# Performance work log

Hardware: AMD Instinct MI355X
Metric: run time of the kernel (lower is better)

The kernel has to match this reference:

```python
import jax, jax.numpy as jnp
import numpy as np

BN_EPS = 1e-5
COS_EPS = 1e-6
LEAKY_SLOPE = 0.01
SIMILARITY_RATIO = 0.5


def setup_inputs() -> dict:
    key = jax.random.key(0)
    ks = jax.random.split(key, 5)
    B, D2, D, M = 2048, 256, 128, 100000
    item_feature = jax.random.normal(ks[0], (B, D2), dtype=jnp.float32)
    all_items = jax.random.normal(ks[1], (M, D), dtype=jnp.float32)
    user_item_id = jax.random.randint(ks[2], (B, 2), 0, M, dtype=jnp.int64)
    W = jax.random.normal(ks[3], (D2, D), dtype=jnp.float32) * (1.0 / np.sqrt(D2))
    b = jax.random.normal(ks[4], (D,), dtype=jnp.float32) * 0.01
    gamma = jnp.ones((D,), dtype=jnp.float32)
    beta = jnp.zeros((D,), dtype=jnp.float32)
    return {"item_feature": item_feature, "all_items": all_items,
            "user_item_id": user_item_id, "W": W, "b": b,
            "gamma": gamma, "beta": beta}


def reference(item_feature, all_items, user_item_id, W, b, gamma, beta):
    # Linear -> BatchNorm1d (training-mode batch stats, biased var) -> LeakyReLU
    h = item_feature @ W + b                       # [B, D]
    mu = jnp.mean(h, axis=0)
    var = jnp.var(h, axis=0)
    hn = (h - mu) * jax.lax.rsqrt(var + BN_EPS) * gamma + beta
    uf = jnp.where(hn >= 0, hn, LEAKY_SLOPE * hn)  # leaky relu

    # dense scoring + top-1 retrieval: [B, M] score matrix
    scores = uf @ all_items.T
    top1 = jnp.argmax(scores, axis=1)              # [B]

    # gather original and retrieved item embeddings
    orig = user_item_id[:, 1]
    a = all_items[orig]                            # [B, D]
    c = all_items[top1]                            # [B, D]

    # cosine similarity (torch CosineSimilarity semantics, eps=1e-6)
    na = jnp.maximum(jnp.sqrt(jnp.sum(a * a, axis=1)), COS_EPS)
    nc = jnp.maximum(jnp.sqrt(jnp.sum(c * c, axis=1)), COS_EPS)
    sim = jnp.sum(a * c, axis=1) / (na * nc)
    sim = (sim + 1.0) * 0.5                        # regularize to [0,1]

    # margin loss against constant labels = similarity_ratio
    labels = jnp.full(sim.shape, SIMILARITY_RATIO, dtype=sim.dtype)
    similarity_loss = jnp.mean(jnp.maximum(sim - labels, 0.0))

    return top1, similarity_loss, jnp.mean(sim)
```

## Files before the change

kernel.cpp:

```cpp
#include <hip/hip_runtime.h>
#include <stdint.h>

#define B_ROWS 2048
#define D2_DIM 256
#define D_DIM 128
#define M_ITEMS 100000
#define M_PAD 100352
#define BN_EPS_F 1e-5f
#define COS_EPS_F 1e-6f
#define LEAKY_F 0.01f

#define BNI 128
#define BK 32
#define SUPER 4

typedef __bf16 bf16x8 __attribute__((ext_vector_type(8)));
typedef float f32x4 __attribute__((ext_vector_type(4)));

__device__ unsigned short g_Aph[B_ROWS * D_DIM];
__device__ unsigned short g_Apl[B_ROWS * D_DIM];
__device__ unsigned short g_Bph[M_PAD * D_DIM];
__device__ unsigned short g_Bpl[M_PAD * D_DIM];

__device__ __forceinline__ unsigned bf16_rne(float f) {
  unsigned u = __float_as_uint(f);
  return (u + 0x7fffu + ((u >> 16) & 1u)) >> 16;
}
__device__ __forceinline__ void split_bf16(float v, unsigned short& hi, unsigned short& lo) {
  unsigned h = bf16_rne(v);
  float hf = __uint_as_float(h << 16);
  unsigned l = bf16_rne(v - hf);
  hi = (unsigned short)h; lo = (unsigned short)l;
}
__device__ __forceinline__ void gload16(const void* g, void* l) {
  __builtin_amdgcn_global_load_lds(
      (const __attribute__((address_space(1))) void*)g,
      (__attribute__((address_space(3))) void*)l, 16, 0, 0);
}

__global__ void k_gemm1(const float* __restrict__ A, const float* __restrict__ W,
                        const float* __restrict__ bias, float* __restrict__ h) {
  __shared__ float arow[D2_DIM];
  const int r = blockIdx.x;
  const int c = threadIdx.x;
  arow[c] = A[r * D2_DIM + c];
  arow[c + 128] = A[r * D2_DIM + c + 128];
  __syncthreads();
  float acc = 0.f;
#pragma unroll 8
  for (int k = 0; k < D2_DIM; k++) acc = fmaf(arow[k], W[k * D_DIM + c], acc);
  h[r * D_DIM + c] = acc + bias[c];
}

__global__ void k_bnstats(const float* __restrict__ h, const float* __restrict__ gamma,
                          const float* __restrict__ beta, float* __restrict__ scale,
                          float* __restrict__ shift) {
  const int c = blockIdx.x;
  const int t = threadIdx.x;
  double s = 0.0, sq = 0.0;
  for (int r = t; r < B_ROWS; r += 256) {
    double v = (double)h[r * D_DIM + c];
    s += v; sq += v * v;
  }
  __shared__ double ls[256], lq[256];
  ls[t] = s; lq[t] = sq;
  __syncthreads();
  for (int off = 128; off; off >>= 1) {
    if (t < off) { ls[t] += ls[t + off]; lq[t] += lq[t + off]; }
    __syncthreads();
  }
  if (t == 0) {
    double mean = ls[0] / (double)B_ROWS;
    double var = lq[0] / (double)B_ROWS - mean * mean;
    float sc = (float)((double)gamma[c] / sqrt(var + (double)BN_EPS_F));
    scale[c] = sc;
    shift[c] = beta[c] - (float)mean * sc;
  }
}

__global__ void k_norm_split(const float* __restrict__ h, const float* __restrict__ scale,
                             const float* __restrict__ shift) {
  int i = blockIdx.x * 256 + threadIdx.x;
  if (i >= B_ROWS * D_DIM) return;
  int c = i & (D_DIM - 1);
  float v = fmaf(h[i], scale[c], shift[c]);
  v = v >= 0.f ? v : LEAKY_F * v;
  unsigned short hi, lo;
  split_bf16(v, hi, lo);
  g_Aph[i] = hi; g_Apl[i] = lo;
}

__global__ void k_build_items(const float* __restrict__ items) {
  long long t = (long long)blockIdx.x * 256 + threadIdx.x;
  long long base = t * 4;
  if (base >= (long long)M_PAD * D_DIM) return;
  float4 v;
  if (base < (long long)M_ITEMS * D_DIM) v = *(const float4*)&items[base];
  else v = make_float4(0.f, 0.f, 0.f, 0.f);
  ushort4 hv, lv;
  split_bf16(v.x, hv.x, lv.x);
  split_bf16(v.y, hv.y, lv.y);
  split_bf16(v.z, hv.z, lv.z);
  split_bf16(v.w, hv.w, lv.w);
  *(ushort4*)&g_Bph[base] = hv;
  *(ushort4*)&g_Bpl[base] = lv;
}

__global__ void k_init(unsigned long long* __restrict__ keys) {
  int i = blockIdx.x * blockDim.x + threadIdx.x;
  if (i < B_ROWS) keys[i] = 0ull;
}

__launch_bounds__(256, 2)
__global__ void k_scores_mfma(unsigned long long* __restrict__ keys) {
  __shared__ __align__(16) char smem[81920];
  char* bufs[3] = { smem, smem + 16384, smem + 32768 };
  char* sAlo = smem + 49152;

  const int tid = threadIdx.x;
  const int l = tid & 63;
  const int w = tid >> 6;
  const int wm = w >> 1;
  const int wn = w & 1;
  const int rowbase = blockIdx.x * 128;
  const int chunk = blockIdx.y * (SUPER * BNI);
  const int lrow = l & 15;
  const int lkg = l >> 4;

  auto STAGEB = [&](int itembase, int ks, char* buf) {
#pragma unroll
    for (int rep = 0; rep < 2; rep++) {
      const int s = tid + rep * 256;
      const size_t goff = (size_t)(itembase + (s >> 2)) * D_DIM + ks
                        + ((s & 3) ^ ((s >> 3) & 3)) * 8;
      gload16(g_Bph + goff, buf + s * 16);
      gload16(g_Bpl + goff, buf + 8192 + s * 16);
    }
  };

#pragma unroll
  for (int rep = 0; rep < 8; rep++) {
    const int s = tid + rep * 256;
    gload16(g_Apl + (size_t)(rowbase + (s >> 4)) * D_DIM
                  + ((s & 15) ^ ((s >> 4) & 15)) * 8,
            sAlo + s * 16);
  }
  bf16x8 ah[4][4];
  {
    const int ar = rowbase + wm * 64 + lrow;
#pragma unroll
    for (int mi = 0; mi < 4; mi++)
#pragma unroll
      for (int kf = 0; kf < 4; kf++)
        ah[mi][kf] = *(const bf16x8*)&g_Aph[(size_t)(ar + mi * 16) * D_DIM + kf * 32 + lkg * 8];
  }
  STAGEB(chunk, 0, bufs[0]);
  STAGEB(chunk, BK, bufs[1]);

  float bestv[16];
  int besti[16];
#pragma unroll
  for (int q = 0; q < 16; q++) { bestv[q] = -3.0e38f; besti[q] = 0x7fffffff; }

  f32x4 acc[4][4];
#pragma unroll
  for (int mi = 0; mi < 4; mi++)
#pragma unroll
    for (int ni = 0; ni < 4; ni++) acc[mi][ni] = (f32x4)(0.0f);

#pragma unroll
  for (int s = 0; s < SUPER; s++) {
    const int itembase = chunk + s * BNI;
#pragma unroll
    for (int kf = 0; kf < 4; kf++) {
      const int j = s * 4 + kf;
      asm volatile("s_waitcnt vmcnt(4)" ::: "memory");
      __builtin_amdgcn_s_barrier();
      {
        const int q = j + 2;
        const int qt = (q >> 2) & (SUPER - 1);
        STAGEB(chunk + qt * BNI, (q & 3) * BK, bufs[q % 3]);
      }
      char* buf = bufs[j % 3];
      bf16x8 bh[4], bl[4], alo[4];
#pragma unroll
      for (int ni = 0; ni < 4; ni++) {
        const int item = wn * 64 + ni * 16 + lrow;
        const int off = (item * 4 + (lkg ^ ((item >> 1) & 3))) * 16;
        bh[ni] = *(const bf16x8*)(buf + off);
        bl[ni] = *(const bf16x8*)(buf + 8192 + off);
      }
#pragma unroll
      for (int mi = 0; mi < 4; mi++) {
        const int row = wm * 64 + mi * 16 + lrow;
        const int off = row * 256 + (((kf * 4 + lkg) ^ (row & 15)) << 4);
        alo[mi] = *(const bf16x8*)(sAlo + off);
      }
      __builtin_amdgcn_s_setprio(1);
#pragma unroll
      for (int mi = 0; mi < 4; mi++)
#pragma unroll
        for (int ni = 0; ni < 4; ni++) {
          f32x4 c = acc[mi][ni];
          c = __builtin_amdgcn_mfma_f32_16x16x32_bf16(ah[mi][kf], bh[ni], c, 0, 0, 0);
          c = __builtin_amdgcn_mfma_f32_16x16x32_bf16(alo[mi], bh[ni], c, 0, 0, 0);
          c = __builtin_amdgcn_mfma_f32_16x16x32_bf16(ah[mi][kf], bl[ni], c, 0, 0, 0);
          acc[mi][ni] = c;
        }
      __builtin_amdgcn_s_setprio(0);
    }
#pragma unroll
    for (int mi = 0; mi < 4; mi++)
#pragma unroll
      for (int ni = 0; ni < 4; ni++) {
        const int col = itembase + wn * 64 + ni * 16 + lrow;
        const bool valid = col < M_ITEMS;
#pragma unroll
        for (int reg = 0; reg < 4; reg++) {
          const float v = acc[mi][ni][reg];
          const int q = mi * 4 + reg;
          if (valid && v > bestv[q]) { bestv[q] = v; besti[q] = col; }
        }
        acc[mi][ni] = (f32x4)(0.0f);
      }
  }
  asm volatile("s_waitcnt vmcnt(0)" ::: "memory");

#pragma unroll
  for (int q = 0; q < 16; q++) {
    float v = bestv[q];
    int bi = besti[q];
#pragma unroll
    for (int off = 1; off < 16; off <<= 1) {
      float ov = __shfl_xor(v, off, 16);
      int oi = __shfl_xor(bi, off, 16);
      if (ov > v || (ov == v && oi < bi)) { v = ov; bi = oi; }
    }
    if (lrow == 0) {
      const int row = rowbase + wm * 64 + (q >> 2) * 16 + lkg * 4 + (q & 3);
      unsigned u = __float_as_uint(v);
      u = (u & 0x80000000u) ? ~u : (u | 0x80000000u);
      unsigned long long key =
          ((unsigned long long)u << 32) | (unsigned)(~(unsigned)bi);
      atomicMax(&keys[row], key);
    }
  }
}

__global__ void k_post(const unsigned long long* __restrict__ keys,
                       const int* __restrict__ uid,
                       const float* __restrict__ items,
                       float* __restrict__ out, float* __restrict__ sims,
                       float* __restrict__ rl) {
  int r = blockIdx.x * blockDim.x + threadIdx.x;
  if (r >= B_ROWS) return;
  unsigned long long key = keys[r];
  int idx = (int)(~(unsigned)(key & 0xFFFFFFFFull));
  out[r] = (float)idx;
  int orig = uid[2 * r + 1];
  const float* a = items + (long long)orig * D_DIM;
  const float* c = items + (long long)idx * D_DIM;
  float aa = 0.f, cc = 0.f, ac = 0.f;
#pragma unroll 4
  for (int d = 0; d < D_DIM; d++) {
    float x = a[d], y = c[d];
    aa = fmaf(x, x, aa);
    cc = fmaf(y, y, cc);
    ac = fmaf(x, y, ac);
  }
  float na = fmaxf(sqrtf(aa), COS_EPS_F);
  float nc = fmaxf(sqrtf(cc), COS_EPS_F);
  float sim = ac / (na * nc);
  sim = (sim + 1.f) * 0.5f;
  sims[r] = sim;
  rl[r] = fmaxf(sim - 0.5f, 0.f);
}

__global__ void k_final(const float* __restrict__ sims, const float* __restrict__ rl,
                        float* __restrict__ out) {
  __shared__ float s1[256], s2[256];
  int t = threadIdx.x;
  float a = 0.f, b = 0.f;
  for (int r = t; r < B_ROWS; r += 256) { a += rl[r]; b += sims[r]; }
  s1[t] = a; s2[t] = b;
  __syncthreads();
  for (int off = 128; off; off >>= 1) {
    if (t < off) { s1[t] += s1[t + off]; s2[t] += s2[t + off]; }
    __syncthreads();
  }
  if (t == 0) {
    out[B_ROWS] = s1[0] / (float)B_ROWS;
    out[B_ROWS + 1] = s2[0] / (float)B_ROWS;
  }
}

extern "C" void kernel_launch(void* const* d_in, const int* in_sizes, int n_in,
                              void* d_out, int out_size, void* d_ws, size_t ws_size,
                              hipStream_t stream) {
  const float* item_feature = (const float*)d_in[0];
  const float* all_items    = (const float*)d_in[1];
  const int*   uid          = (const int*)d_in[2];
  const float* W            = (const float*)d_in[3];
  const float* bias         = (const float*)d_in[4];
  const float* gamma        = (const float*)d_in[5];
  const float* beta         = (const float*)d_in[6];
  float* out = (float*)d_out;

  float* h     = (float*)d_ws;
  float* scale = h + B_ROWS * D_DIM;
  float* shift = scale + D_DIM;
  unsigned long long* keys = (unsigned long long*)(shift + D_DIM);
  float* sims  = (float*)(keys + B_ROWS);
  float* rl    = sims + B_ROWS;

  k_gemm1<<<B_ROWS, D_DIM, 0, stream>>>(item_feature, W, bias, h);
  k_bnstats<<<D_DIM, 256, 0, stream>>>(h, gamma, beta, scale, shift);
  k_norm_split<<<(B_ROWS * D_DIM + 255) / 256, 256, 0, stream>>>(h, scale, shift);
  k_build_items<<<(M_PAD * D_DIM / 4 + 255) / 256, 256, 0, stream>>>(all_items);
  k_init<<<(B_ROWS + 255) / 256, 256, 0, stream>>>(keys);
  dim3 sg(B_ROWS / 128, M_PAD / (SUPER * BNI));
  k_scores_mfma<<<sg, 256, 0, stream>>>(keys);
  k_post<<<(B_ROWS + 255) / 256, 256, 0, stream>>>(keys, uid, all_items, out, sims, rl);
  k_final<<<1, 256, 0, stream>>>(sims, rl, out);
}
```

Measured before the change: 282.8 us.

## Switch to double-buffered 64-wide K stages and load A-low directly from global

The B-tile pipeline changes from a triple buffer with 32-wide K steps and a partial vmcnt wait to a double buffer with 64-wide K steps and a full vmcnt(0) wait before each barrier. The A low-part tile is no longer kept in LDS; it is reloaded from global memory (cache) every step into registers. The intent is to halve the barrier count, cut LDS use so more can stay resident, and raise work per stage. In exchange, prefetch overlap is shallower because every stage waits for all outstanding loads, and the per-step global A loads add latency and register pressure.

```diff
diff --git a/kernel.cpp b/kernel.cpp
--- a/kernel.cpp
+++ b/kernel.cpp
@@ -11,8 +11,9 @@
 #define LEAKY_F 0.01f
 
 #define BNI 128
-#define BK 32
+#define BKS 64
 #define SUPER 4
+#define NSTEPS 8
 
 typedef __bf16 bf16x8 __attribute__((ext_vector_type(8)));
 typedef float f32x4 __attribute__((ext_vector_type(4)));
@@ -113,9 +114,8 @@
 
 __launch_bounds__(256, 2)
 __global__ void k_scores_mfma(unsigned long long* __restrict__ keys) {
-  __shared__ __align__(16) char smem[81920];
-  char* bufs[3] = { smem, smem + 16384, smem + 32768 };
-  char* sAlo = smem + 49152;
+  __shared__ __align__(16) char smem[65536];
+  char* bufs[2] = { smem, smem + 32768 };
 
   const int tid = threadIdx.x;
   const int l = tid & 63;
@@ -129,33 +129,23 @@
 
   auto STAGEB = [&](int itembase, int ks, char* buf) {
 #pragma unroll
-    for (int rep = 0; rep < 2; rep++) {
+    for (int rep = 0; rep < 4; rep++) {
       const int s = tid + rep * 256;
-      const size_t goff = (size_t)(itembase + (s >> 2)) * D_DIM + ks
-                        + ((s & 3) ^ ((s >> 3) & 3)) * 8;
+      const size_t goff = (size_t)(itembase + (s >> 3)) * D_DIM + ks
+                        + (((s & 7) ^ ((s >> 3) & 7)) * 8);
       gload16(g_Bph + goff, buf + s * 16);
-      gload16(g_Bpl + goff, buf + 8192 + s * 16);
+      gload16(g_Bpl + goff, buf + 16384 + s * 16);
     }
   };
 
-#pragma unroll
-  for (int rep = 0; rep < 8; rep++) {
-    const int s = tid + rep * 256;
-    gload16(g_Apl + (size_t)(rowbase + (s >> 4)) * D_DIM
-                  + ((s & 15) ^ ((s >> 4) & 15)) * 8,
-            sAlo + s * 16);
-  }
+  STAGEB(chunk, 0, bufs[0]);
   bf16x8 ah[4][4];
-  {
-    const int ar = rowbase + wm * 64 + lrow;
-#pragma unroll
-    for (int mi = 0; mi < 4; mi++)
-#pragma unroll
-      for (int kf = 0; kf < 4; kf++)
-        ah[mi][kf] = *(const bf16x8*)&g_Aph[(size_t)(ar + mi * 16) * D_DIM + kf * 32 + lkg * 8];
-  }
-  STAGEB(chunk, 0, bufs[0]);
-  STAGEB(chunk, BK, bufs[1]);
+  const int ar = rowbase + wm * 64 + lrow;
+#pragma unroll
+  for (int mi = 0; mi < 4; mi++)
+#pragma unroll
+    for (int kf = 0; kf < 4; kf++)
+      ah[mi][kf] = *(const bf16x8*)&g_Aph[(size_t)(ar + mi * 16) * D_DIM + kf * 32 + lkg * 8];
 
   float bestv[16];
   int besti[16];
@@ -172,42 +162,47 @@
   for (int s = 0; s < SUPER; s++) {
     const int itembase = chunk + s * BNI;
 #pragma unroll
-    for (int kf = 0; kf < 4; kf++) {
-      const int j = s * 4 + kf;
-      asm volatile("s_waitcnt vmcnt(4)" ::: "memory");
+    for (int khalf = 0; khalf < 2; khalf++) {
+      const int j = s * 2 + khalf;
+      asm volatile("s_waitcnt vmcnt(0)" ::: "memory");
       __builtin_amdgcn_s_barrier();
-      {
-        const int q = j + 2;
-        const int qt = (q >> 2) & (SUPER - 1);
-        STAGEB(chunk + qt * BNI, (q & 3) * BK, bufs[q % 3]);
+      if (j < NSTEPS - 1) {
+        const int q = j + 1;
+        STAGEB(chunk + (q >> 1) * BNI, (q & 1) * BKS, bufs[q & 1]);
       }
-      char* buf = bufs[j % 3];
-      bf16x8 bh[4], bl[4], alo[4];
-#pragma unroll
-      for (int ni = 0; ni < 4; ni++) {
-        const int item = wn * 64 + ni * 16 + lrow;
-        const int off = (item * 4 + (lkg ^ ((item >> 1) & 3))) * 16;
-        bh[ni] = *(const bf16x8*)(buf + off);
-        bl[ni] = *(const bf16x8*)(buf + 8192 + off);
+      bf16x8 alo0[4], alo1[4];
+#pragma unroll
+      for (int mi = 0; mi < 4; mi++) {
+        const size_t abase = (size_t)(ar + mi * 16) * D_DIM + khalf * 64 + lkg * 8;
+        alo0[mi] = *(const bf16x8*)&g_Apl[abase];
+        alo1[mi] = *(const bf16x8*)&g_Apl[abase + 32];
       }
-#pragma unroll
-      for (int mi = 0; mi < 4; mi++) {
-        const int row = wm * 64 + mi * 16 + lrow;
-        const int off = row * 256 + (((kf * 4 + lkg) ^ (row & 15)) << 4);
-        alo[mi] = *(const bf16x8*)(sAlo + off);
+      char* buf = bufs[j & 1];
+#pragma unroll
+      for (int kk = 0; kk < 2; kk++) {
+        const int kf = khalf * 2 + kk;
+        bf16x8 bh[4], bl[4];
+#pragma unroll
+        for (int ni = 0; ni < 4; ni++) {
+          const int item = wn * 64 + ni * 16 + lrow;
+          const int q8 = kk * 4 + lkg;
+          const int off = (item * 8 + (q8 ^ (item & 7))) * 16;
+          bh[ni] = *(const bf16x8*)(buf + off);
+          bl[ni] = *(const bf16x8*)(buf + 16384 + off);
+        }
+        __builtin_amdgcn_s_setprio(1);
+#pragma unroll
+        for (int mi = 0; mi < 4; mi++)
+#pragma unroll
+          for (int ni = 0; ni < 4; ni++) {
+            f32x4 c = acc[mi][ni];
+            c = __builtin_amdgcn_mfma_f32_16x16x32_bf16(ah[mi][kf], bh[ni], c, 0, 0, 0);
+            c = __builtin_amdgcn_mfma_f32_16x16x32_bf16(kk ? alo1[mi] : alo0[mi], bh[ni], c, 0, 0, 0);
+            c = __builtin_amdgcn_mfma_f32_16x16x32_bf16(ah[mi][kf], bl[ni], c, 0, 0, 0);
+            acc[mi][ni] = c;
+          }
+        __builtin_amdgcn_s_setprio(0);
       }
-      __builtin_amdgcn_s_setprio(1);
-#pragma unroll
-      for (int mi = 0; mi < 4; mi++)
-#pragma unroll
-        for (int ni = 0; ni < 4; ni++) {
-          f32x4 c = acc[mi][ni];
-          c = __builtin_amdgcn_mfma_f32_16x16x32_bf16(ah[mi][kf], bh[ni], c, 0, 0, 0);
-          c = __builtin_amdgcn_mfma_f32_16x16x32_bf16(alo[mi], bh[ni], c, 0, 0, 0);
-          c = __builtin_amdgcn_mfma_f32_16x16x32_bf16(ah[mi][kf], bl[ni], c, 0, 0, 0);
-          acc[mi][ni] = c;
-        }
-      __builtin_amdgcn_s_setprio(0);
     }
 #pragma unroll
     for (int mi = 0; mi < 4; mi++)
@@ -224,7 +219,6 @@
         acc[mi][ni] = (f32x4)(0.0f);
       }
   }
-  asm volatile("s_waitcnt vmcnt(0)" ::: "memory");
 
 #pragma unroll
   for (int q = 0; q < 16; q++) {
```

Result: slower. 395.1 us (+39.7%).
